# Performance work log

Hardware: AMD Instinct MI355X
Metric: run time of the kernel (lower is better)

The kernel has to match this reference:

```python
import jax, jax.numpy as jnp
import numpy as np

N = 50000      # total atoms in batched graph
E = 800000     # edges
IN = 128       # in_feats
OUT = 64       # out_feats (per GAT head)
H = 4          # num_heads
NEG_SLOPE = 0.2
BN_EPS = 1e-5


def setup_inputs() -> dict:
    key = jax.random.key(0)
    ks = jax.random.split(key, 16)
    s = 0.1  # keep activations well-scaled
    return {
        "node_feats": jax.random.normal(ks[0], (N, IN), jnp.float32),
        "W_fc":       jax.random.normal(ks[1], (IN, H * OUT), jnp.float32) * s,
        "attn_l":     jax.random.normal(ks[2], (H, OUT), jnp.float32) * s,
        "attn_r":     jax.random.normal(ks[3], (H, OUT), jnp.float32) * s,
        "gat_res_w":  jax.random.normal(ks[4], (IN, H * OUT), jnp.float32) * s,
        "gat_bias":   jax.random.normal(ks[5], (H * OUT,), jnp.float32) * s,
        "conv_w":     jax.random.normal(ks[6], (1, H, 1), jnp.float32) * s,
        "conv_b":     jax.random.normal(ks[7], (1,), jnp.float32) * s,
        "res_w":      jax.random.normal(ks[8], (IN, OUT), jnp.float32) * s,
        "res_b":      jax.random.normal(ks[9], (OUT,), jnp.float32) * s,
        "bn_gamma":   jnp.ones((OUT,), jnp.float32),
        "bn_beta":    jnp.zeros((OUT,), jnp.float32),
        "src":        jax.random.randint(ks[10], (E,), 0, N, jnp.int32),
        "dst":        jax.random.randint(ks[11], (E,), 0, N, jnp.int32),
        "etype":      0,
    }


def reference(node_feats, W_fc, attn_l, attn_r, gat_res_w, gat_bias,
              conv_w, conv_b, res_w, res_b, bn_gamma, bn_beta,
              src, dst, etype):
    # ---- GATConv (DGL semantics, eval mode: no dropout) ----
    h = (node_feats @ W_fc).reshape(-1, H, OUT)            # [N,H,D]
    el = jnp.sum(h * attn_l, axis=-1)                      # [N,H]
    er = jnp.sum(h * attn_r, axis=-1)                      # [N,H]
    e = jax.nn.leaky_relu(el[src] + er[dst], NEG_SLOPE)    # [E,H]
    # segment softmax over incoming edges of each dst node
    m = jax.ops.segment_max(e, dst, num_segments=N)        # [N,H]
    m = jnp.where(jnp.isfinite(m), m, 0.0)                 # empty segments
    a = jnp.exp(e - m[dst])                                # [E,H]
    ssum = jax.ops.segment_sum(a, dst, num_segments=N)     # [N,H]
    alpha = a / (ssum[dst] + 1e-16)                        # [E,H]
    # weighted aggregation: rst[v] = sum_{(u->v)} alpha * h[u]
    rst = jax.ops.segment_sum(alpha[:, :, None] * h[src], dst, num_segments=N)  # [N,H,D]
    # GAT residual (in != H*OUT -> linear res_fc, no bias) + bias + activation
    rst = rst + (node_feats @ gat_res_w).reshape(-1, H, OUT) + gat_bias.reshape(H, OUT)
    rst = jax.nn.relu(rst)                                 # [N,H,D]
    # ---- Conv1d(4 -> 1, kernel=1): weighted head merge ----
    y = jnp.einsum("nhd,h->nd", rst, conv_w[0, :, 0]) + conv_b[0]  # [N,D]
    # ---- outer residual ----
    y = y + jax.nn.relu(node_feats @ res_w + res_b)
    # ---- BatchNorm1d (training-style batch stats) ----
    mean = jnp.mean(y, axis=0)
    var = jnp.var(y, axis=0)
    return (y - mean) / jnp.sqrt(var + BN_EPS) * bn_gamma + bn_beta
```

## Files before the change

kernel.cpp:

```cpp
#include <hip/hip_runtime.h>

#define IN_F   128
#define OUTD   64
#define HOUT   256
#define NEG_SLOPE 0.2f
#define BN_EPS 1e-5f
#define HIST_BLOCKS 512
#define BPAD 136

typedef __attribute__((ext_vector_type(8))) short bf16x8;
typedef __attribute__((ext_vector_type(4))) float f32x4;
typedef __attribute__((ext_vector_type(2))) float f32x2;

__device__ __forceinline__ unsigned short f2bf(float f) {
    union { float f; unsigned u; } v; v.f = f;
    unsigned r = (v.u + 0x7FFF + ((v.u >> 16) & 1)) >> 16;
    return (unsigned short)r;
}
__device__ __forceinline__ float bf2f(unsigned short h) {
    union { unsigned u; float f; } v; v.u = ((unsigned)h) << 16;
    return v.f;
}

__global__ __launch_bounds__(256) void k0_pack(
    const float* __restrict__ W_fc, const float* __restrict__ W_gres,
    const float* __restrict__ W_res, unsigned short* __restrict__ Btg)
{
    int idx = blockIdx.x * 256 + threadIdx.x;
    if (idx >= 576 * 128) return;
    int c = idx >> 7, k = idx & 127;
    float v;
    if (c < 256)      v = W_fc[k * HOUT + c];
    else if (c < 512) v = W_gres[k * HOUT + (c - 256)];
    else              v = W_res[k * OUTD + (c - 512)];
    Btg[idx] = f2bf(v);
}

__global__ __launch_bounds__(256) void k1_gemm(
    const float* __restrict__ A, const unsigned short* __restrict__ Btg,
    const float* __restrict__ attn_l, const float* __restrict__ attn_r,
    const float* __restrict__ gat_bias, const float* __restrict__ res_b,
    const int* __restrict__ dst, int* __restrict__ degree, int* __restrict__ rank,
    unsigned char* __restrict__ Hh8, unsigned char* __restrict__ Hr8,
    unsigned short* __restrict__ Rres,
    float* __restrict__ el, float* __restrict__ er,
    int N, int E, int Mtiles)
{
    __shared__ __align__(16) unsigned short As[64 * BPAD];
    __shared__ __align__(16) unsigned short Bs[64 * BPAD];
    int bid = blockIdx.x, t = threadIdx.x;

    if (bid >= Mtiles) {
        int hb = bid - Mtiles;
        for (int e = hb * 256 + t; e < E; e += HIST_BLOCKS * 256)
            rank[e] = atomicAdd(degree + dst[e], 1);
        return;
    }

    int m0 = bid * 64;

    for (int i = 0; i < 8; ++i) {
        int slot = t + i * 256;
        int r = slot >> 5, c4 = (slot & 31) << 2;
        float4 v = make_float4(0.f, 0.f, 0.f, 0.f);
        if (m0 + r < N) v = *(const float4*)(A + (size_t)(m0 + r) * IN_F + c4);
        ushort4 o;
        o.x = f2bf(v.x); o.y = f2bf(v.y); o.z = f2bf(v.z); o.w = f2bf(v.w);
        *(ushort4*)(&As[r * BPAD + c4]) = o;
    }

    int w = t >> 6, lane = t & 63, quad = lane >> 4, n15 = lane & 15;
    bf16x8 af[4];
    unsigned hpack[4][4] = {};
    unsigned rpack[4][4] = {};

    for (int n = 0; n < 9; ++n) {
        if (n) __syncthreads();
        for (int i = 0; i < 4; ++i) {
            int slot = t + i * 256;
            int c = slot >> 4, k0 = (slot & 15) << 3;
            *(uint4*)(&Bs[c * BPAD + k0]) = *(const uint4*)(Btg + (size_t)(n * 64 + c) * IN_F + k0);
        }
        __syncthreads();
        if (n == 0) {
#pragma unroll
            for (int ks = 0; ks < 4; ++ks)
                af[ks] = *(const bf16x8*)(&As[(w * 16 + n15) * BPAD + ks * 32 + quad * 8]);
        }

        f32x4 acc[4] = {};
#pragma unroll
        for (int ks = 0; ks < 4; ++ks) {
            bf16x8 bfr[4];
#pragma unroll
            for (int j = 0; j < 4; ++j)
                bfr[j] = *(const bf16x8*)(&Bs[(j * 16 + n15) * BPAD + ks * 32 + quad * 8]);
#pragma unroll
            for (int j = 0; j < 4; ++j)
                acc[j] = __builtin_amdgcn_mfma_f32_16x16x32_bf16(af[ks], bfr[j], acc[j], 0, 0, 0);
        }

        if (n < 4) {
            float alv[4], arv[4];
#pragma unroll
            for (int j = 0; j < 4; ++j) {
                alv[j] = attn_l[n * 64 + j * 16 + n15];
                arv[j] = attn_r[n * 64 + j * 16 + n15];
            }
#pragma unroll
            for (int reg = 0; reg < 4; ++reg) {
                float pl = acc[0][reg] * alv[0] + acc[1][reg] * alv[1]
                         + acc[2][reg] * alv[2] + acc[3][reg] * alv[3];
                float pr = acc[0][reg] * arv[0] + acc[1][reg] * arv[1]
                         + acc[2][reg] * arv[2] + acc[3][reg] * arv[3];
#pragma unroll
                for (int off = 1; off < 16; off <<= 1) {
                    pl += __shfl_xor(pl, off);
                    pr += __shfl_xor(pr, off);
                }
                int r = m0 + w * 16 + quad * 4 + reg;
                if (n15 == 0 && r < N) {
                    el[(size_t)r * 4 + n] = pl;
                    er[(size_t)r * 4 + n] = pr;
                }
            }
#pragma unroll
            for (int j = 0; j < 4; ++j)
#pragma unroll
                for (int reg = 0; reg < 4; ++reg) {
                    float v = acc[j][reg];
                    unsigned pk = (unsigned)__builtin_amdgcn_cvt_pk_fp8_f32(v, v, 0, false);
                    hpack[j][reg] |= (pk & 0xffu) << (8 * n);
                }
        } else if (n < 8) {
            int hd = n - 4;
            float bv[4];
#pragma unroll
            for (int j = 0; j < 4; ++j) bv[j] = gat_bias[hd * 64 + j * 16 + n15];
#pragma unroll
            for (int j = 0; j < 4; ++j)
#pragma unroll
                for (int reg = 0; reg < 4; ++reg) {
                    float v = acc[j][reg] + bv[j];
                    unsigned pk = (unsigned)__builtin_amdgcn_cvt_pk_fp8_f32(v, v, 0, false);
                    rpack[j][reg] |= (pk & 0xffu) << (8 * hd);
                }
        } else {
            float bv[4];
#pragma unroll
            for (int j = 0; j < 4; ++j) bv[j] = res_b[j * 16 + n15];
#pragma unroll
            for (int reg = 0; reg < 4; ++reg) {
                int r = m0 + w * 16 + quad * 4 + reg;
                if (r < N) {
#pragma unroll
                    for (int j = 0; j < 4; ++j)
                        Rres[(size_t)r * OUTD + j * 16 + n15] = f2bf(acc[j][reg] + bv[j]);
                }
            }
        }
    }

#pragma unroll
    for (int reg = 0; reg < 4; ++reg) {
        int r = m0 + w * 16 + quad * 4 + reg;
        if (r < N) {
#pragma unroll
            for (int j = 0; j < 4; ++j) {
                *(unsigned*)(Hh8 + ((size_t)r << 8) + (j * 16 + n15) * 4) = hpack[j][reg];
                *(unsigned*)(Hr8 + ((size_t)r << 8) + (j * 16 + n15) * 4) = rpack[j][reg];
            }
        }
    }
}

__global__ __launch_bounds__(256) void scanA_kernel(const int* __restrict__ degree,
                                                    int* __restrict__ excl,
                                                    int* __restrict__ blocksum, int N) {
    __shared__ int sm[256];
    int t = threadIdx.x;
    int i = blockIdx.x * 256 + t;
    int d = (i < N) ? degree[i] : 0;
    sm[t] = d; __syncthreads();
    for (int off = 1; off < 256; off <<= 1) {
        int v = (t >= off) ? sm[t - off] : 0;
        __syncthreads();
        sm[t] += v;
        __syncthreads();
    }
    if (i < N) excl[i] = sm[t] - d;
    if (t == 255) blocksum[blockIdx.x] = sm[255];
}

__global__ __launch_bounds__(256) void scanB_kernel(const int* __restrict__ blocksum,
                                                    int* __restrict__ base, int nb) {
    __shared__ int sm[256];
    int t = threadIdx.x;
    int d = (t < nb) ? blocksum[t] : 0;
    sm[t] = d; __syncthreads();
    for (int off = 1; off < 256; off <<= 1) {
        int v = (t >= off) ? sm[t - off] : 0;
        __syncthreads();
        sm[t] += v;
        __syncthreads();
    }
    if (t < nb) base[t] = sm[t] - d;
}

__global__ void scatter_kernel(const int* __restrict__ src, const int* __restrict__ dst,
                               const int* __restrict__ rank, const int* __restrict__ excl,
                               const int* __restrict__ base,
                               const float* __restrict__ el, const float* __restrict__ er,
                               uint4* __restrict__ es_sorted, int E) {
    int e = blockIdx.x * 256 + threadIdx.x;
    if (e >= E) return;
    int d = dst[e], u = src[e];
    int p = excl[d] + base[d >> 8] + rank[e];
    float4 l = *(const float4*)(el + (size_t)u * 4);
    float4 r = *(const float4*)(er + (size_t)d * 4);
    float x, s0, s1, s2, s3;
    x = l.x + r.x; x = x > 0.f ? x : NEG_SLOPE * x; s0 = __expf(x);
    x = l.y + r.y; x = x > 0.f ? x : NEG_SLOPE * x; s1 = __expf(x);
    x = l.z + r.z; x = x > 0.f ? x : NEG_SLOPE * x; s2 = __expf(x);
    x = l.w + r.w; x = x > 0.f ? x : NEG_SLOPE * x; s3 = __expf(x);
    uint4 o;
    o.x = (unsigned)u << 8;
    o.y = (unsigned)f2bf(s0) | ((unsigned)f2bf(s1) << 16);
    o.z = (unsigned)f2bf(s2) | ((unsigned)f2bf(s3) << 16);
    o.w = 0u;
    es_sorted[p] = o;
}

__global__ __launch_bounds__(256) void agg_kernel(
    const unsigned char* __restrict__ Hh8, const unsigned char* __restrict__ Hr8,
    const unsigned short* __restrict__ Rres,
    const int* __restrict__ excl, const int* __restrict__ base,
    const uint4* __restrict__ es_sorted,
    const float* __restrict__ conv_w, const float* __restrict__ conv_b,
    float* __restrict__ y, int N, int E)
{
    int wave = threadIdx.x >> 6, lane = threadIdx.x & 63;
    int v = blockIdx.x * 4 + wave;
    if (v >= N) return;
    int b  = excl[v] + base[v >> 8];
    int e2 = (v + 1 < N) ? (excl[v + 1] + base[(v + 1) >> 8]) : E;
    int deg = e2 - b;

    const unsigned char* hbase = Hh8 + lane * 4;
    float a0 = 0.f, a1 = 0.f, a2 = 0.f, a3 = 0.f;
    float p0 = 0.f, p1 = 0.f, p2 = 0.f, p3 = 0.f;

    for (int i0 = 0; i0 < deg; i0 += 64) {
        int j = i0 + lane;
        uint4 es = make_uint4(0u, 0u, 0u, 0u);
        if (j < deg) es = es_sorted[b + j];
        p0 += bf2f((unsigned short)(es.y & 0xffff));
        p1 += bf2f((unsigned short)(es.y >> 16));
        p2 += bf2f((unsigned short)(es.z & 0xffff));
        p3 += bf2f((unsigned short)(es.z >> 16));
        int cl = deg - i0; if (cl > 64) cl = 64;
        int jj = 0;
        for (; jj + 1 < cl; jj += 2) {
            unsigned uA   = (unsigned)__builtin_amdgcn_readlane((int)es.x, jj);
            unsigned sA01 = (unsigned)__builtin_amdgcn_readlane((int)es.y, jj);
            unsigned sA23 = (unsigned)__builtin_amdgcn_readlane((int)es.z, jj);
            unsigned uB   = (unsigned)__builtin_amdgcn_readlane((int)es.x, jj + 1);
            unsigned sB01 = (unsigned)__builtin_amdgcn_readlane((int)es.y, jj + 1);
            unsigned sB23 = (unsigned)__builtin_amdgcn_readlane((int)es.z, jj + 1);
            unsigned hvA = *(const unsigned*)(hbase + uA);
            unsigned hvB = *(const unsigned*)(hbase + uB);
            f32x2 loA = __builtin_amdgcn_cvt_pk_f32_fp8(hvA, false);
            f32x2 hiA = __builtin_amdgcn_cvt_pk_f32_fp8(hvA, true);
            f32x2 loB = __builtin_amdgcn_cvt_pk_f32_fp8(hvB, false);
            f32x2 hiB = __builtin_amdgcn_cvt_pk_f32_fp8(hvB, true);
            a0 += bf2f((unsigned short)(sA01 & 0xffff)) * loA.x;
            a1 += bf2f((unsigned short)(sA01 >> 16))    * loA.y;
            a2 += bf2f((unsigned short)(sA23 & 0xffff)) * hiA.x;
            a3 += bf2f((unsigned short)(sA23 >> 16))    * hiA.y;
            a0 += bf2f((unsigned short)(sB01 & 0xffff)) * loB.x;
            a1 += bf2f((unsigned short)(sB01 >> 16))    * loB.y;
            a2 += bf2f((unsigned short)(sB23 & 0xffff)) * hiB.x;
            a3 += bf2f((unsigned short)(sB23 >> 16))    * hiB.y;
        }
        if (jj < cl) {
            unsigned uA   = (unsigned)__builtin_amdgcn_readlane((int)es.x, jj);
            unsigned sA01 = (unsigned)__builtin_amdgcn_readlane((int)es.y, jj);
            unsigned sA23 = (unsigned)__builtin_amdgcn_readlane((int)es.z, jj);
            unsigned hvA = *(const unsigned*)(hbase + uA);
            f32x2 loA = __builtin_amdgcn_cvt_pk_f32_fp8(hvA, false);
            f32x2 hiA = __builtin_amdgcn_cvt_pk_f32_fp8(hvA, true);
            a0 += bf2f((unsigned short)(sA01 & 0xffff)) * loA.x;
            a1 += bf2f((unsigned short)(sA01 >> 16))    * loA.y;
            a2 += bf2f((unsigned short)(sA23 & 0xffff)) * hiA.x;
            a3 += bf2f((unsigned short)(sA23 >> 16))    * hiA.y;
        }
    }
#pragma unroll
    for (int off = 1; off < 64; off <<= 1) {
        p0 += __shfl_xor(p0, off); p1 += __shfl_xor(p1, off);
        p2 += __shfl_xor(p2, off); p3 += __shfl_xor(p3, off);
    }
    float r0 = 1.f / (p0 + 1e-16f), r1 = 1.f / (p1 + 1e-16f);
    float r2 = 1.f / (p2 + 1e-16f), r3 = 1.f / (p3 + 1e-16f);

    unsigned hr = *(const unsigned*)(Hr8 + ((size_t)v << 8) + lane * 4);
    f32x2 rlo = __builtin_amdgcn_cvt_pk_f32_fp8(hr, false);
    f32x2 rhi = __builtin_amdgcn_cvt_pk_f32_fp8(hr, true);
    float resv = bf2f(Rres[(size_t)v * OUTD + lane]);
    float yv = conv_b[0] + (resv > 0.f ? resv : 0.f);
    float tt;
    tt = a0 * r0 + rlo.x; tt = tt > 0.f ? tt : 0.f; yv += conv_w[0] * tt;
    tt = a1 * r1 + rlo.y; tt = tt > 0.f ? tt : 0.f; yv += conv_w[1] * tt;
    tt = a2 * r2 + rhi.x; tt = tt > 0.f ? tt : 0.f; yv += conv_w[2] * tt;
    tt = a3 * r3 + rhi.y; tt = tt > 0.f ? tt : 0.f; yv += conv_w[3] * tt;
    y[(size_t)v * OUTD + lane] = yv;
}

__global__ __launch_bounds__(256) void bn_partial_kernel(const float* __restrict__ y,
                                                         float* __restrict__ bnsum,
                                                         float* __restrict__ bnsumsq, int total) {
    __shared__ float smem[256];
    int t = threadIdx.x;
    size_t idx = (size_t)blockIdx.x * 256 + t;
    size_t stride = (size_t)gridDim.x * 256;
    float sum = 0.f, sq = 0.f;
    for (; idx < (size_t)total; idx += stride) {
        float v = y[idx];
        sum += v; sq += v * v;
    }
    int d = t & 63;
    smem[t] = sum; __syncthreads();
    if (t < 64) atomicAdd(bnsum + d, smem[t] + smem[t + 64] + smem[t + 128] + smem[t + 192]);
    __syncthreads();
    smem[t] = sq; __syncthreads();
    if (t < 64) atomicAdd(bnsumsq + d, smem[t] + smem[t + 64] + smem[t + 128] + smem[t + 192]);
}

__global__ void norm_kernel(const float* __restrict__ y,
                            const float* __restrict__ bnsum, const float* __restrict__ bnsumsq,
                            const float* __restrict__ gamma, const float* __restrict__ beta,
                            float* __restrict__ out, int total4, float invN) {
    int idx = blockIdx.x * blockDim.x + threadIdx.x;
    if (idx >= total4) return;
    float4 v = *(const float4*)(y + (size_t)idx * 4);
    int d = (idx * 4) & 63;
    float4 o;
#pragma unroll
    for (int k = 0; k < 4; ++k) {
        float mean = bnsum[d + k] * invN;
        float var = bnsumsq[d + k] * invN - mean * mean;
        float sc = gamma[d + k] * rsqrtf(var + BN_EPS);
        float sh = beta[d + k] - mean * sc;
        (&o.x)[k] = (&v.x)[k] * sc + sh;
    }
    *(float4*)(out + (size_t)idx * 4) = o;
}

extern "C" void kernel_launch(void* const* d_in, const int* in_sizes, int n_in,
                              void* d_out, int out_size, void* d_ws, size_t ws_size,
                              hipStream_t stream) {
    const float* node_feats = (const float*)d_in[0];
    const float* W_fc       = (const float*)d_in[1];
    const float* attn_l     = (const float*)d_in[2];
    const float* attn_r     = (const float*)d_in[3];
    const float* gat_res_w  = (const float*)d_in[4];
    const float* gat_bias   = (const float*)d_in[5];
    const float* conv_w     = (const float*)d_in[6];
    const float* conv_b     = (const float*)d_in[7];
    const float* res_w      = (const float*)d_in[8];
    const float* res_b      = (const float*)d_in[9];
    const float* bn_gamma   = (const float*)d_in[10];
    const float* bn_beta    = (const float*)d_in[11];
    const int*   src        = (const int*)d_in[12];
    const int*   dst        = (const int*)d_in[13];

    const int N = in_sizes[0] / IN_F;
    const int E = in_sizes[12];
    const int Mtiles = (N + 63) / 64;
    const int nb = (N + 255) / 256;

    char* ws = (char*)d_ws;
    size_t off = 0;
    auto alloc = [&](size_t bytes) -> void* {
        void* p = (void*)(ws + off);
        off += (bytes + 255) & ~(size_t)255;
        return p;
    };

    int*   degree  = (int*)alloc((size_t)N * 4);
    float* bnsum   = (float*)alloc(64 * 4);
    float* bnsumsq = (float*)alloc(64 * 4);
    size_t zero_bytes = off;
    int*            rank      = (int*)alloc((size_t)E * 4);
    int*            excl      = (int*)alloc((size_t)N * 4);
    int*            blocksum  = (int*)alloc(256 * 4);
    int*            base      = (int*)alloc(256 * 4);
    uint4*          es_sorted = (uint4*)alloc((size_t)E * 16);
    unsigned short* Btg       = (unsigned short*)alloc((size_t)576 * IN_F * 2);
    unsigned char*  Hh8       = (unsigned char*)alloc((size_t)N * 256);
    unsigned char*  Hr8       = (unsigned char*)alloc((size_t)N * 256);
    unsigned short* Rres      = (unsigned short*)alloc((size_t)N * OUTD * 2);
    float*          el        = (float*)alloc((size_t)N * 4 * 4);
    float*          er        = (float*)alloc((size_t)N * 4 * 4);
    float*          y         = (float*)alloc((size_t)N * OUTD * 4);
    (void)ws_size; (void)n_in; (void)out_size;

    hipMemsetAsync(d_ws, 0, zero_bytes, stream);

    k0_pack<<<(576 * 128 + 255) / 256, 256, 0, stream>>>(W_fc, gat_res_w, res_w, Btg);
    k1_gemm<<<Mtiles + HIST_BLOCKS, 256, 0, stream>>>(node_feats, Btg, attn_l, attn_r,
                                                      gat_bias, res_b, dst, degree, rank,
                                                      Hh8, Hr8, Rres, el, er, N, E, Mtiles);
    scanA_kernel<<<nb, 256, 0, stream>>>(degree, excl, blocksum, N);
    scanB_kernel<<<1, 256, 0, stream>>>(blocksum, base, nb);
    scatter_kernel<<<(E + 255) / 256, 256, 0, stream>>>(src, dst, rank, excl, base,
                                                        el, er, es_sorted, E);
    agg_kernel<<<(N + 3) / 4, 256, 0, stream>>>(Hh8, Hr8, Rres, excl, base, es_sorted,
                                                conv_w, conv_b, y, N, E);
    bn_partial_kernel<<<512, 256, 0, stream>>>(y, bnsum, bnsumsq, N * OUTD);
    norm_kernel<<<(N * OUTD / 4 + 255) / 256, 256, 0, stream>>>(y, bnsum, bnsumsq,
                                                                bn_gamma, bn_beta, (float*)d_out,
                                                                N * OUTD / 4, 1.f / (float)N);
}
```

Baseline: 271.2 us.

## Make GEMM persistent with full weight in LDS and fold attention into extra columns

Rewrites the projection GEMM as a persistent kernel of 256 blocks of 512 threads. Each block loads the whole swizzled bf16 weight matrix into LDS once, then each wave loops over 32-row tiles, reading A directly into registers instead of reloading B from global memory for every 64-row tile. The el/er attention projections are precomputed as W_fc·attn columns appended to the weight matrix, replacing per-tile shuffle reductions with one extra MFMA column block. The degree histogram now runs at the end of each wave instead of in separate blocks. This costs about 148KB of LDS per block, so occupancy is limited, and the atomics are serialized after the GEMM work.

```diff
diff --git a/kernel.cpp b/kernel.cpp
--- a/kernel.cpp
+++ b/kernel.cpp
@@ -5,8 +5,10 @@
 #define HOUT   256
 #define NEG_SLOPE 0.2f
 #define BN_EPS 1e-5f
-#define HIST_BLOCKS 512
-#define BPAD 136
+#define NCOLS  592
+#define GEMM_BLOCKS 256
+#define K1_THREADS 512
+#define K1_WAVES 8
 
 typedef __attribute__((ext_vector_type(8))) short bf16x8;
 typedef __attribute__((ext_vector_type(4))) float f32x4;
@@ -24,154 +26,186 @@
 
 __global__ __launch_bounds__(256) void k0_pack(
     const float* __restrict__ W_fc, const float* __restrict__ W_gres,
-    const float* __restrict__ W_res, unsigned short* __restrict__ Btg)
+    const float* __restrict__ W_res,
+    const float* __restrict__ attn_l, const float* __restrict__ attn_r,
+    unsigned short* __restrict__ Btg)
 {
-    int idx = blockIdx.x * 256 + threadIdx.x;
-    if (idx >= 576 * 128) return;
-    int c = idx >> 7, k = idx & 127;
-    float v;
-    if (c < 256)      v = W_fc[k * HOUT + c];
-    else if (c < 512) v = W_gres[k * HOUT + (c - 256)];
-    else              v = W_res[k * OUTD + (c - 512)];
-    Btg[idx] = f2bf(v);
-}
-
-__global__ __launch_bounds__(256) void k1_gemm(
+    int bid = blockIdx.x, t = threadIdx.x;
+    if (bid < 288) {
+        int idx = bid * 256 + t;
+        int c = idx >> 7, k = idx & 127;
+        float v;
+        if (c < 256)      v = W_fc[k * HOUT + c];
+        else if (c < 512) v = W_gres[k * HOUT + (c - 256)];
+        else              v = W_res[k * OUTD + (c - 512)];
+        Btg[idx] = f2bf(v);
+        return;
+    }
+    for (int p = t; p < 512; p += 256) {
+        int h = p >> 7, k = p & 127;
+        float sl = 0.f, sr = 0.f;
+        for (int d = 0; d < 64; ++d) {
+            float wv = W_fc[k * HOUT + h * 64 + d];
+            sl += wv * attn_l[h * 64 + d];
+            sr += wv * attn_r[h * 64 + d];
+        }
+        Btg[(576 + h) * 128 + k] = f2bf(sl);
+        Btg[(580 + h) * 128 + k] = f2bf(sr);
+    }
+    for (int idx = t; idx < 8 * 128; idx += 256)
+        Btg[584 * 128 + idx] = 0;
+}
+
+__global__ __launch_bounds__(512, 2) void k1_gemm(
     const float* __restrict__ A, const unsigned short* __restrict__ Btg,
-    const float* __restrict__ attn_l, const float* __restrict__ attn_r,
     const float* __restrict__ gat_bias, const float* __restrict__ res_b,
     const int* __restrict__ dst, int* __restrict__ degree, int* __restrict__ rank,
     unsigned char* __restrict__ Hh8, unsigned char* __restrict__ Hr8,
     unsigned short* __restrict__ Rres,
     float* __restrict__ el, float* __restrict__ er,
-    int N, int E, int Mtiles)
+    int N, int E)
 {
-    __shared__ __align__(16) unsigned short As[64 * BPAD];
-    __shared__ __align__(16) unsigned short Bs[64 * BPAD];
-    int bid = blockIdx.x, t = threadIdx.x;
-
-    if (bid >= Mtiles) {
-        int hb = bid - Mtiles;
-        for (int e = hb * 256 + t; e < E; e += HIST_BLOCKS * 256)
-            rank[e] = atomicAdd(degree + dst[e], 1);
-        return;
-    }
-
-    int m0 = bid * 64;
-
-    for (int i = 0; i < 8; ++i) {
-        int slot = t + i * 256;
-        int r = slot >> 5, c4 = (slot & 31) << 2;
-        float4 v = make_float4(0.f, 0.f, 0.f, 0.f);
-        if (m0 + r < N) v = *(const float4*)(A + (size_t)(m0 + r) * IN_F + c4);
-        ushort4 o;
-        o.x = f2bf(v.x); o.y = f2bf(v.y); o.z = f2bf(v.z); o.w = f2bf(v.w);
-        *(ushort4*)(&As[r * BPAD + c4]) = o;
-    }
-
+    __shared__ __align__(16) unsigned short Bsh[NCOLS * 128];
+    int t = threadIdx.x;
     int w = t >> 6, lane = t & 63, quad = lane >> 4, n15 = lane & 15;
-    bf16x8 af[4];
-    unsigned hpack[4][4] = {};
-    unsigned rpack[4][4] = {};
-
-    for (int n = 0; n < 9; ++n) {
-        if (n) __syncthreads();
-        for (int i = 0; i < 4; ++i) {
-            int slot = t + i * 256;
-            int c = slot >> 4, k0 = (slot & 15) << 3;
-            *(uint4*)(&Bs[c * BPAD + k0]) = *(const uint4*)(Btg + (size_t)(n * 64 + c) * IN_F + k0);
-        }
-        __syncthreads();
-        if (n == 0) {
-#pragma unroll
-            for (int ks = 0; ks < 4; ++ks)
-                af[ks] = *(const bf16x8*)(&As[(w * 16 + n15) * BPAD + ks * 32 + quad * 8]);
-        }
-
-        f32x4 acc[4] = {};
+
+    for (int slot = t; slot < NCOLS * 16; slot += K1_THREADS) {
+        int c = slot >> 4, ch = slot & 15;
+        uint4 v = *(const uint4*)(Btg + c * 128 + ch * 8);
+        *(uint4*)(&Bsh[c * 128 + ((ch ^ (c & 15)) << 3)]) = v;
+    }
+    __syncthreads();
+
+    float gbv[4][4], rbv[4];
+#pragma unroll
+    for (int hd = 0; hd < 4; ++hd)
+#pragma unroll
+        for (int j = 0; j < 4; ++j) gbv[hd][j] = gat_bias[hd * 64 + j * 16 + n15];
+#pragma unroll
+    for (int j = 0; j < 4; ++j) rbv[j] = res_b[j * 16 + n15];
+
+    int chs[4];
+#pragma unroll
+    for (int ks = 0; ks < 4; ++ks) chs[ks] = (((ks << 2) + quad) ^ n15) << 3;
+
+    int gw = blockIdx.x * K1_WAVES + w;
+    int T = (N + 31) / 32;
+    for (int task = gw; task < T; task += GEMM_BLOCKS * K1_WAVES) {
+        int m0 = task * 32;
+
+        bf16x8 af[2][4];
+#pragma unroll
+        for (int i = 0; i < 2; ++i) {
+            int r = m0 + i * 16 + n15;
+#pragma unroll
+            for (int ks = 0; ks < 4; ++ks) {
+                float4 v0 = make_float4(0.f, 0.f, 0.f, 0.f), v1 = v0;
+                if (r < N) {
+                    const float* ap = A + (size_t)r * IN_F + ks * 32 + quad * 8;
+                    v0 = *(const float4*)ap;
+                    v1 = *(const float4*)(ap + 4);
+                }
+                bf16x8 o;
+                o[0] = f2bf(v0.x); o[1] = f2bf(v0.y); o[2] = f2bf(v0.z); o[3] = f2bf(v0.w);
+                o[4] = f2bf(v1.x); o[5] = f2bf(v1.y); o[6] = f2bf(v1.z); o[7] = f2bf(v1.w);
+                af[i][ks] = o;
+            }
+        }
+
+        unsigned hpack[2][4][4] = {};
+        unsigned rpack[2][4][4] = {};
+
+        for (int n = 0; n < 9; ++n) {
+            f32x4 acc[2][4] = {};
+#pragma unroll
+            for (int ks = 0; ks < 4; ++ks) {
+                bf16x8 bfr[4];
+#pragma unroll
+                for (int j = 0; j < 4; ++j) {
+                    int col = n * 64 + j * 16 + n15;
+                    bfr[j] = *(const bf16x8*)(&Bsh[col * 128 + chs[ks]]);
+                }
+#pragma unroll
+                for (int i = 0; i < 2; ++i)
+#pragma unroll
+                    for (int j = 0; j < 4; ++j)
+                        acc[i][j] = __builtin_amdgcn_mfma_f32_16x16x32_bf16(af[i][ks], bfr[j], acc[i][j], 0, 0, 0);
+            }
+            if (n < 4) {
+#pragma unroll
+                for (int i = 0; i < 2; ++i)
+#pragma unroll
+                    for (int j = 0; j < 4; ++j)
+#pragma unroll
+                        for (int reg = 0; reg < 4; ++reg) {
+                            float v = acc[i][j][reg];
+                            unsigned pk = (unsigned)__builtin_amdgcn_cvt_pk_fp8_f32(v, v, 0, false);
+                            hpack[i][j][reg] |= (pk & 0xffu) << (8 * n);
+                        }
+            } else if (n < 8) {
+                int hd = n - 4;
+#pragma unroll
+                for (int i = 0; i < 2; ++i)
+#pragma unroll
+                    for (int j = 0; j < 4; ++j)
+#pragma unroll
+                        for (int reg = 0; reg < 4; ++reg) {
+                            float v = acc[i][j][reg] + gbv[hd][j];
+                            unsigned pk = (unsigned)__builtin_amdgcn_cvt_pk_fp8_f32(v, v, 0, false);
+                            rpack[i][j][reg] |= (pk & 0xffu) << (8 * hd);
+                        }
+            } else {
+#pragma unroll
+                for (int i = 0; i < 2; ++i)
+#pragma unroll
+                    for (int reg = 0; reg < 4; ++reg) {
+                        int r = m0 + i * 16 + quad * 4 + reg;
+                        if (r < N) {
+#pragma unroll
+                            for (int j = 0; j < 4; ++j)
+                                Rres[(size_t)r * OUTD + j * 16 + n15] = f2bf(acc[i][j][reg] + rbv[j]);
+                        }
+                    }
+            }
+        }
+
+        f32x4 acc2[2] = {};
 #pragma unroll
         for (int ks = 0; ks < 4; ++ks) {
-            bf16x8 bfr[4];
-#pragma unroll
-            for (int j = 0; j < 4; ++j)
-                bfr[j] = *(const bf16x8*)(&Bs[(j * 16 + n15) * BPAD + ks * 32 + quad * 8]);
-#pragma unroll
-            for (int j = 0; j < 4; ++j)
-                acc[j] = __builtin_amdgcn_mfma_f32_16x16x32_bf16(af[ks], bfr[j], acc[j], 0, 0, 0);
-        }
-
-        if (n < 4) {
-            float alv[4], arv[4];
-#pragma unroll
-            for (int j = 0; j < 4; ++j) {
-                alv[j] = attn_l[n * 64 + j * 16 + n15];
-                arv[j] = attn_r[n * 64 + j * 16 + n15];
-            }
+            int col = 576 + n15;
+            bf16x8 b = *(const bf16x8*)(&Bsh[col * 128 + chs[ks]]);
+            acc2[0] = __builtin_amdgcn_mfma_f32_16x16x32_bf16(af[0][ks], b, acc2[0], 0, 0, 0);
+            acc2[1] = __builtin_amdgcn_mfma_f32_16x16x32_bf16(af[1][ks], b, acc2[1], 0, 0, 0);
+        }
+#pragma unroll
+        for (int i = 0; i < 2; ++i)
 #pragma unroll
             for (int reg = 0; reg < 4; ++reg) {
-                float pl = acc[0][reg] * alv[0] + acc[1][reg] * alv[1]
-                         + acc[2][reg] * alv[2] + acc[3][reg] * alv[3];
-                float pr = acc[0][reg] * arv[0] + acc[1][reg] * arv[1]
-                         + acc[2][reg] * arv[2] + acc[3][reg] * arv[3];
-#pragma unroll
-                for (int off = 1; off < 16; off <<= 1) {
-                    pl += __shfl_xor(pl, off);
-                    pr += __shfl_xor(pr, off);
-                }
-                int r = m0 + w * 16 + quad * 4 + reg;
-                if (n15 == 0 && r < N) {
-                    el[(size_t)r * 4 + n] = pl;
-                    er[(size_t)r * 4 + n] = pr;
+                int r = m0 + i * 16 + quad * 4 + reg;
+                if (r < N && n15 < 8) {
+                    float v = acc2[i][reg];
+                    if (n15 < 4) el[(size_t)r * 4 + n15] = v;
+                    else         er[(size_t)r * 4 + (n15 - 4)] = v;
                 }
             }
-#pragma unroll
-            for (int j = 0; j < 4; ++j)
-#pragma unroll
-                for (int reg = 0; reg < 4; ++reg) {
-                    float v = acc[j][reg];
-                    unsigned pk = (unsigned)__builtin_amdgcn_cvt_pk_fp8_f32(v, v, 0, false);
-                    hpack[j][reg] |= (pk & 0xffu) << (8 * n);
-                }
-        } else if (n < 8) {
-            int hd = n - 4;
-            float bv[4];
-#pragma unroll
-            for (int j = 0; j < 4; ++j) bv[j] = gat_bias[hd * 64 + j * 16 + n15];
-#pragma unroll
-            for (int j = 0; j < 4; ++j)
-#pragma unroll
-                for (int reg = 0; reg < 4; ++reg) {
-                    float v = acc[j][reg] + bv[j];
-                    unsigned pk = (unsigned)__builtin_amdgcn_cvt_pk_fp8_f32(v, v, 0, false);
-                    rpack[j][reg] |= (pk & 0xffu) << (8 * hd);
-                }
-        } else {
-            float bv[4];
-#pragma unroll
-            for (int j = 0; j < 4; ++j) bv[j] = res_b[j * 16 + n15];
+
+#pragma unroll
+        for (int i = 0; i < 2; ++i)
 #pragma unroll
             for (int reg = 0; reg < 4; ++reg) {
-                int r = m0 + w * 16 + quad * 4 + reg;
+                int r = m0 + i * 16 + quad * 4 + reg;
                 if (r < N) {
 #pragma unroll
-                    for (int j = 0; j < 4; ++j)
-                        Rres[(size_t)r * OUTD + j * 16 + n15] = f2bf(acc[j][reg] + bv[j]);
+                    for (int j = 0; j < 4; ++j) {
+                        *(unsigned*)(Hh8 + ((size_t)r << 8) + (j * 16 + n15) * 4) = hpack[i][j][reg];
+                        *(unsigned*)(Hr8 + ((size_t)r << 8) + (j * 16 + n15) * 4) = rpack[i][j][reg];
+                    }
                 }
             }
-        }
-    }
-
-#pragma unroll
-    for (int reg = 0; reg < 4; ++reg) {
-        int r = m0 + w * 16 + quad * 4 + reg;
-        if (r < N) {
-#pragma unroll
-            for (int j = 0; j < 4; ++j) {
-                *(unsigned*)(Hh8 + ((size_t)r << 8) + (j * 16 + n15) * 4) = hpack[j][reg];
-                *(unsigned*)(Hr8 + ((size_t)r << 8) + (j * 16 + n15) * 4) = rpack[j][reg];
-            }
-        }
-    }
+    }
+
+    for (int e = gw * 64 + lane; e < E; e += GEMM_BLOCKS * K1_WAVES * 64)
+        rank[e] = atomicAdd(degree + dst[e], 1);
 }
 
 __global__ __launch_bounds__(256) void scanA_kernel(const int* __restrict__ degree,
@@ -376,7 +410,6 @@
 
     const int N = in_sizes[0] / IN_F;
     const int E = in_sizes[12];
-    const int Mtiles = (N + 63) / 64;
     const int nb = (N + 255) / 256;
 
     char* ws = (char*)d_ws;
@@ -396,7 +429,7 @@
     int*            blocksum  = (int*)alloc(256 * 4);
     int*            base      = (int*)alloc(256 * 4);
     uint4*          es_sorted = (uint4*)alloc((size_t)E * 16);
-    unsigned short* Btg       = (unsigned short*)alloc((size_t)576 * IN_F * 2);
+    unsigned short* Btg       = (unsigned short*)alloc((size_t)NCOLS * IN_F * 2);
     unsigned char*  Hh8       = (unsigned char*)alloc((size_t)N * 256);
     unsigned char*  Hr8       = (unsigned char*)alloc((size_t)N * 256);
     unsigned short* Rres      = (unsigned short*)alloc((size_t)N * OUTD * 2);
@@ -407,10 +440,10 @@
 
     hipMemsetAsync(d_ws, 0, zero_bytes, stream);
 
-    k0_pack<<<(576 * 128 + 255) / 256, 256, 0, stream>>>(W_fc, gat_res_w, res_w, Btg);
-    k1_gemm<<<Mtiles + HIST_BLOCKS, 256, 0, stream>>>(node_feats, Btg, attn_l, attn_r,
-                                                      gat_bias, res_b, dst, degree, rank,
-                                                      Hh8, Hr8, Rres, el, er, N, E, Mtiles);
+    k0_pack<<<289, 256, 0, stream>>>(W_fc, gat_res_w, res_w, attn_l, attn_r, Btg);
+    k1_gemm<<<GEMM_BLOCKS, K1_THREADS, 0, stream>>>(node_feats, Btg, gat_bias, res_b,
+                                                    dst, degree, rank, Hh8, Hr8, Rres,
+                                                    el, er, N, E);
     scanA_kernel<<<nb, 256, 0, stream>>>(degree, excl, blocksum, N);
     scanB_kernel<<<1, 256, 0, stream>>>(blocksum, base, nb);
     scatter_kernel<<<(E + 255) / 256, 256, 0, stream>>>(src, dst, rank, excl, base,
```

Measured after the change: 307.8 us. +13.5%, slower.
